# Kernel tuning notes

Measured on AMD Instinct MI355X. Metric: run time of the kernel, lower is better.

Reference implementation:

```python
import jax, jax.numpy as jnp
import numpy as np

B, S, D = 524288, 10, 6  # batch of independent tiny attention problems; original module is one [10,6] sample


def setup_inputs() -> dict:
    key = jax.random.key(0)
    ks = jax.random.split(key, 7)
    bound = 1.0 / np.sqrt(D)  # torch nn.Linear default init range
    x = jax.random.normal(ks[0], (B, S, D), dtype=jnp.float32)
    Wk = jax.random.uniform(ks[1], (D, D), jnp.float32, -bound, bound)
    bk = jax.random.uniform(ks[2], (D,), jnp.float32, -bound, bound)
    Wq = jax.random.uniform(ks[3], (D, D), jnp.float32, -bound, bound)
    bq = jax.random.uniform(ks[4], (D,), jnp.float32, -bound, bound)
    Wv = jax.random.uniform(ks[5], (D, D), jnp.float32, -bound, bound)
    bv = jax.random.uniform(ks[6], (D,), jnp.float32, -bound, bound)
    return {"x": x, "Wk": Wk, "bk": bk, "Wq": Wq, "bq": bq, "Wv": Wv, "bv": bv}


def reference(x, Wk, bk, Wq, bq, Wv, bv):
    # Linear layers (torch stores W as [out,in]; y = x W^T + b)
    k = jnp.einsum('bsd,ed->bse', x, Wk) + bk  # [B,S,D]
    q = jnp.einsum('bsd,ed->bse', x, Wq) + bq
    v = jnp.einsum('bsd,ed->bse', x, Wv) + bv
    # per-query attention over the 10 keys (no scaling in original)
    scores = jax.nn.softmax(jnp.einsum('bqd,bkd->bqk', q, k), axis=-1)  # [B,S,S]
    out = jnp.einsum('bqk,bkd->bqd', scores, v)  # [B,S,D]
    # original sums attended vector over feature dim -> one scalar per query
    return jnp.sum(out, axis=-1)  # [B,S]
```

## Files before the change

kernel.cpp:

```cpp
#include <hip/hip_runtime.h>


#define NB 524288
#define S 10
#define D 6
#define TPB 256
#define EPB 128
#define XFL (S * D)
#define LDS_FLOATS (EPB * XFL)

__global__ void precompute_kernel(const float* __restrict__ Wk, const float* __restrict__ bk,
                                  const float* __restrict__ Wq, const float* __restrict__ bq,
                                  const float* __restrict__ Wv, const float* __restrict__ bv,
                                  float* __restrict__ ws) {
    const float LOG2E = 1.44269504088896340736f;
    int t = threadIdx.x;
    if (t < 36) {
        int d = t / 6, dp = t % 6;
        float g = 0.f;
        for (int e = 0; e < D; ++e) g += Wq[e * D + d] * Wk[e * D + dp];
        ws[t] = g * LOG2E;
    } else if (t < 42) {
        int dp = t - 36;
        float s = 0.f;
        for (int e = 0; e < D; ++e) s += bq[e] * Wk[e * D + dp];
        ws[t] = s * LOG2E;
    } else if (t < 48) {
        int d = t - 42;
        float s = 0.f;
        for (int e = 0; e < D; ++e) s += Wv[e * D + d];
        ws[t] = s;
    } else if (t == 48) {
        float s = 0.f;
        for (int e = 0; e < D; ++e) s += bv[e];
        ws[t] = s;
    }
}

__device__ __forceinline__ float sconst(const float* __restrict__ p, int i) {
    return __int_as_float(__builtin_amdgcn_readfirstlane(__float_as_int(p[i])));
}

__global__ __launch_bounds__(TPB, 4) void attn_kernel(const float* __restrict__ x,
                                                      const float* __restrict__ ws,
                                                      float* __restrict__ out) {
    __shared__ float xs[LDS_FLOATS];
    const int t = threadIdx.x;
    const int blk = blockIdx.x;
    const int wave = t >> 6;
    const int lane = t & 63;

    const float* gbase = x + (size_t)blk * LDS_FLOATS;
    #pragma unroll
    for (int i = 0; i < 8; ++i) {
        int c = wave + 4 * i;
        if (c < 30) {
            __builtin_amdgcn_global_load_lds(
                (const __attribute__((address_space(1))) void*)(gbase + c * 256 + lane * 4),
                (__attribute__((address_space(3))) void*)(&xs[c * 256 + lane * 4]),
                16, 0, 0);
        }
    }

    float G[36], w[6], wvs[6];
    #pragma unroll
    for (int i = 0; i < 36; ++i) G[i] = sconst(ws, i);
    #pragma unroll
    for (int i = 0; i < 6; ++i) w[i] = sconst(ws, 36 + i);
    #pragma unroll
    for (int i = 0; i < 6; ++i) wvs[i] = sconst(ws, 42 + i);
    const float bvs = sconst(ws, 48);

    __syncthreads();

    const int e = t >> 1;
    const int h = t & 1;
    const float* xe = &xs[e * XFL];

    float xv[XFL];
    const float4* xr = (const float4*)xe;
    #pragma unroll
    for (int i = 0; i < 15; ++i) {
        float4 v = xr[i];
        xv[4 * i + 0] = v.x;
        xv[4 * i + 1] = v.y;
        xv[4 * i + 2] = v.z;
        xv[4 * i + 3] = v.w;
    }

    const float* xq0 = xe + h * (5 * D);
    float tq[5][6];
    #pragma unroll
    for (int j = 0; j < 5; ++j) {
        float xq[6];
        #pragma unroll
        for (int d = 0; d < 6; ++d) xq[d] = xq0[j * 6 + d];
        #pragma unroll
        for (int dp = 0; dp < 6; ++dp) {
            float s = 0.f;
            #pragma unroll
            for (int d = 0; d < 6; ++d) s += xq[d] * G[d * 6 + dp];
            tq[j][dp] = s;
        }
    }

    float num[5] = {0.f, 0.f, 0.f, 0.f, 0.f};
    float den[5] = {0.f, 0.f, 0.f, 0.f, 0.f};
    #pragma unroll
    for (int k = 0; k < S; ++k) {
        float a = 0.f, vk = bvs;
        #pragma unroll
        for (int d = 0; d < 6; ++d) {
            a += w[d] * xv[k * 6 + d];
            vk += wvs[d] * xv[k * 6 + d];
        }
        #pragma unroll
        for (int j = 0; j < 5; ++j) {
            float s = a;
            #pragma unroll
            for (int d = 0; d < 6; ++d) s += tq[j][d] * xv[k * 6 + d];
            float ex = __builtin_amdgcn_exp2f(s);
            den[j] += ex;
            num[j] += ex * vk;
        }
    }

    float* op = out + (size_t)blk * (EPB * S) + t * 5;
    #pragma unroll
    for (int j = 0; j < 5; ++j) op[j] = num[j] * __builtin_amdgcn_rcpf(den[j]);
}

extern "C" void kernel_launch(void* const* d_in, const int* in_sizes, int n_in,
                              void* d_out, int out_size, void* d_ws, size_t ws_size,
                              hipStream_t stream) {
    const float* x  = (const float*)d_in[0];
    const float* Wk = (const float*)d_in[1];
    const float* bk = (const float*)d_in[2];
    const float* Wq = (const float*)d_in[3];
    const float* bq = (const float*)d_in[4];
    const float* Wv = (const float*)d_in[5];
    const float* bv = (const float*)d_in[6];
    float* out = (float*)d_out;
    float* ws  = (float*)d_ws;

    precompute_kernel<<<1, 64, 0, stream>>>(Wk, bk, Wq, bq, Wv, bv, ws);
    attn_kernel<<<NB / EPB, TPB, 0, stream>>>(x, ws, out);
}
```

Before: 43.64 us.

## Double-buffer x tiles in LDS across a per-block tile loop and coalesce outputs

Each block now runs 128 threads and loops over 8 tiles of 64 elements. While the current tile is computed, the next tile is prefetched with async global-to-LDS loads into a second buffer, so memory traffic overlaps compute. Results are staged through LDS so each output store is fully coalesced. The grid becomes much smaller (1024 blocks of 2 waves), which lowers occupancy and latency hiding on a kernel that is already close to bandwidth-bound. The loop also adds extra barriers per tile.

After: 45.08 us. +3.3%, slower.

```diff
diff --git a/kernel.cpp b/kernel.cpp
--- a/kernel.cpp
+++ b/kernel.cpp
@@ -4,10 +4,11 @@
 #define NB 524288
 #define S 10
 #define D 6
-#define TPB 256
-#define EPB 128
+#define TPB 128
+#define EPT 64
+#define TILES 8
 #define XFL (S * D)
-#define LDS_FLOATS (EPB * XFL)
+#define TFL (EPT * XFL)
 
 __global__ void precompute_kernel(const float* __restrict__ Wk, const float* __restrict__ bk,
                                   const float* __restrict__ Wq, const float* __restrict__ bq,
@@ -41,26 +42,29 @@
     return __int_as_float(__builtin_amdgcn_readfirstlane(__float_as_int(p[i])));
 }
 
+__device__ __forceinline__ void stage_tile(const float* __restrict__ gsrc,
+                                           float* __restrict__ ldst,
+                                           int wave, int lane) {
+    #pragma unroll
+    for (int i = 0; i < 8; ++i) {
+        int c = wave + 2 * i;
+        if (c < 15) {
+            __builtin_amdgcn_global_load_lds(
+                (const __attribute__((address_space(1))) void*)(gsrc + c * 256 + lane * 4),
+                (__attribute__((address_space(3))) void*)(ldst + c * 256 + lane * 4),
+                16, 0, 0);
+        }
+    }
+}
+
 __global__ __launch_bounds__(TPB, 4) void attn_kernel(const float* __restrict__ x,
                                                       const float* __restrict__ ws,
                                                       float* __restrict__ out) {
-    __shared__ float xs[LDS_FLOATS];
+    __shared__ float xs[2][TFL];
     const int t = threadIdx.x;
-    const int blk = blockIdx.x;
     const int wave = t >> 6;
     const int lane = t & 63;
-
-    const float* gbase = x + (size_t)blk * LDS_FLOATS;
-    #pragma unroll
-    for (int i = 0; i < 8; ++i) {
-        int c = wave + 4 * i;
-        if (c < 30) {
-            __builtin_amdgcn_global_load_lds(
-                (const __attribute__((address_space(1))) void*)(gbase + c * 256 + lane * 4),
-                (__attribute__((address_space(3))) void*)(&xs[c * 256 + lane * 4]),
-                16, 0, 0);
-        }
-    }
+    const int blk = blockIdx.x;
 
     float G[36], w[6], wvs[6];
     #pragma unroll
@@ -71,63 +75,80 @@
     for (int i = 0; i < 6; ++i) wvs[i] = sconst(ws, 42 + i);
     const float bvs = sconst(ws, 48);
 
-    __syncthreads();
+    const float* gbase = x + (size_t)blk * (TILES * TFL);
+    stage_tile(gbase, &xs[0][0], wave, lane);
 
-    const int e = t >> 1;
-    const int h = t & 1;
-    const float* xe = &xs[e * XFL];
+    #pragma unroll 2
+    for (int tt = 0; tt < TILES; ++tt) {
+        __syncthreads();
 
-    float xv[XFL];
-    const float4* xr = (const float4*)xe;
-    #pragma unroll
-    for (int i = 0; i < 15; ++i) {
-        float4 v = xr[i];
-        xv[4 * i + 0] = v.x;
-        xv[4 * i + 1] = v.y;
-        xv[4 * i + 2] = v.z;
-        xv[4 * i + 3] = v.w;
-    }
+        const float* xe = &xs[tt & 1][(t >> 1) * XFL];
 
-    const float* xq0 = xe + h * (5 * D);
-    float tq[5][6];
-    #pragma unroll
-    for (int j = 0; j < 5; ++j) {
-        float xq[6];
+        float xv[XFL];
+        const float4* xr = (const float4*)xe;
         #pragma unroll
-        for (int d = 0; d < 6; ++d) xq[d] = xq0[j * 6 + d];
-        #pragma unroll
-        for (int dp = 0; dp < 6; ++dp) {
-            float s = 0.f;
-            #pragma unroll
-            for (int d = 0; d < 6; ++d) s += xq[d] * G[d * 6 + dp];
-            tq[j][dp] = s;
+        for (int i = 0; i < 15; ++i) {
+            float4 v = xr[i];
+            xv[4 * i + 0] = v.x;
+            xv[4 * i + 1] = v.y;
+            xv[4 * i + 2] = v.z;
+            xv[4 * i + 3] = v.w;
         }
-    }
 
-    float num[5] = {0.f, 0.f, 0.f, 0.f, 0.f};
-    float den[5] = {0.f, 0.f, 0.f, 0.f, 0.f};
-    #pragma unroll
-    for (int k = 0; k < S; ++k) {
-        float a = 0.f, vk = bvs;
-        #pragma unroll
-        for (int d = 0; d < 6; ++d) {
-            a += w[d] * xv[k * 6 + d];
-            vk += wvs[d] * xv[k * 6 + d];
-        }
+        const float* xq0 = xe + (t & 1) * (5 * D);
+        float tq[5][6];
         #pragma unroll
         for (int j = 0; j < 5; ++j) {
-            float s = a;
+            float xq[6];
             #pragma unroll
-            for (int d = 0; d < 6; ++d) s += tq[j][d] * xv[k * 6 + d];
-            float ex = __builtin_amdgcn_exp2f(s);
-            den[j] += ex;
-            num[j] += ex * vk;
+            for (int d = 0; d < 6; ++d) xq[d] = xq0[j * 6 + d];
+            #pragma unroll
+            for (int dp = 0; dp < 6; ++dp) {
+                float s = 0.f;
+                #pragma unroll
+                for (int d = 0; d < 6; ++d) s += xq[d] * G[d * 6 + dp];
+                tq[j][dp] = s;
+            }
         }
+
+        if (tt + 1 < TILES)
+            stage_tile(gbase + (size_t)(tt + 1) * TFL, &xs[(tt + 1) & 1][0], wave, lane);
+
+        float num[5] = {0.f, 0.f, 0.f, 0.f, 0.f};
+        float den[5] = {0.f, 0.f, 0.f, 0.f, 0.f};
+        #pragma unroll
+        for (int k = 0; k < S; ++k) {
+            float a = 0.f, vk = bvs;
+            #pragma unroll
+            for (int d = 0; d < 6; ++d) {
+                a += w[d] * xv[k * 6 + d];
+                vk += wvs[d] * xv[k * 6 + d];
+            }
+            #pragma unroll
+            for (int j = 0; j < 5; ++j) {
+                float s = a;
+                #pragma unroll
+                for (int d = 0; d < 6; ++d) s += tq[j][d] * xv[k * 6 + d];
+                float ex = __builtin_amdgcn_exp2f(s);
+                den[j] += ex;
+                num[j] += ex * vk;
+            }
+        }
+
+        __syncthreads();
+
+        float* os = &xs[tt & 1][0];
+        #pragma unroll
+        for (int j = 0; j < 5; ++j)
+            os[t * 5 + j] = num[j] * __builtin_amdgcn_rcpf(den[j]);
+
+        __syncthreads();
+
+        float* ob = out + (size_t)(blk * TILES + tt) * (EPT * S);
+        #pragma unroll
+        for (int i = 0; i < 5; ++i)
+            ob[i * TPB + t] = os[i * TPB + t];
     }
-
-    float* op = out + (size_t)blk * (EPB * S) + t * 5;
-    #pragma unroll
-    for (int j = 0; j < 5; ++j) op[j] = num[j] * __builtin_amdgcn_rcpf(den[j]);
 }
 
 extern "C" void kernel_launch(void* const* d_in, const int* in_sizes, int n_in,
@@ -144,5 +165,5 @@
     float* ws  = (float*)d_ws;
 
     precompute_kernel<<<1, 64, 0, stream>>>(Wk, bk, Wq, bq, Wv, bv, ws);
-    attn_kernel<<<NB / EPB, TPB, 0, stream>>>(x, ws, out);
+    attn_kernel<<<NB / (EPT * TILES), TPB, 0, stream>>>(x, ws, out);
 }
```

## Fuse weight precompute into attention kernel and halve block size

Applied to the files above, without the earlier changes.

Removes the separate single-block precompute launch. Each block now recomputes the folded Wq·Wk matrix, the bias projection and the Wv sums from the raw weights and pins them to scalar registers. Block size drops to 128 threads covering 64 elements, so there are twice as many blocks and each does a smaller LDS staging. The cost is redundant per-block weight loads and about 250 FMAs per thread, traded against the launch gap and the dependency between two kernels.

Result: slower. 50.38 us (+15.4%).

```diff
diff --git a/kernel.cpp b/kernel.cpp
--- a/kernel.cpp
+++ b/kernel.cpp
@@ -4,57 +4,33 @@
 #define NB 524288
 #define S 10
 #define D 6
-#define TPB 256
-#define EPB 128
+#define TPB 128
+#define EPB 64
 #define XFL (S * D)
 #define LDS_FLOATS (EPB * XFL)
 
-__global__ void precompute_kernel(const float* __restrict__ Wk, const float* __restrict__ bk,
-                                  const float* __restrict__ Wq, const float* __restrict__ bq,
-                                  const float* __restrict__ Wv, const float* __restrict__ bv,
-                                  float* __restrict__ ws) {
-    const float LOG2E = 1.44269504088896340736f;
-    int t = threadIdx.x;
-    if (t < 36) {
-        int d = t / 6, dp = t % 6;
-        float g = 0.f;
-        for (int e = 0; e < D; ++e) g += Wq[e * D + d] * Wk[e * D + dp];
-        ws[t] = g * LOG2E;
-    } else if (t < 42) {
-        int dp = t - 36;
-        float s = 0.f;
-        for (int e = 0; e < D; ++e) s += bq[e] * Wk[e * D + dp];
-        ws[t] = s * LOG2E;
-    } else if (t < 48) {
-        int d = t - 42;
-        float s = 0.f;
-        for (int e = 0; e < D; ++e) s += Wv[e * D + d];
-        ws[t] = s;
-    } else if (t == 48) {
-        float s = 0.f;
-        for (int e = 0; e < D; ++e) s += bv[e];
-        ws[t] = s;
-    }
+__device__ __forceinline__ float pin(float v) {
+    return __int_as_float(__builtin_amdgcn_readfirstlane(__float_as_int(v)));
 }
 
-__device__ __forceinline__ float sconst(const float* __restrict__ p, int i) {
-    return __int_as_float(__builtin_amdgcn_readfirstlane(__float_as_int(p[i])));
-}
-
-__global__ __launch_bounds__(TPB, 4) void attn_kernel(const float* __restrict__ x,
-                                                      const float* __restrict__ ws,
-                                                      float* __restrict__ out) {
+__global__ __launch_bounds__(TPB, 4) void attn_fused(const float* __restrict__ x,
+                                                     const float* __restrict__ Wk,
+                                                     const float* __restrict__ Wq,
+                                                     const float* __restrict__ bq,
+                                                     const float* __restrict__ Wv,
+                                                     const float* __restrict__ bv,
+                                                     float* __restrict__ out) {
     __shared__ float xs[LDS_FLOATS];
     const int t = threadIdx.x;
-    const int blk = blockIdx.x;
     const int wave = t >> 6;
     const int lane = t & 63;
+    const int blk = blockIdx.x;
 
     const float* gbase = x + (size_t)blk * LDS_FLOATS;
     #pragma unroll
     for (int i = 0; i < 8; ++i) {
-        int c = wave + 4 * i;
-        if (c < 30) {
+        int c = wave + 2 * i;
+        if (c < 15) {
             __builtin_amdgcn_global_load_lds(
                 (const __attribute__((address_space(1))) void*)(gbase + c * 256 + lane * 4),
                 (__attribute__((address_space(3))) void*)(&xs[c * 256 + lane * 4]),
@@ -62,19 +38,46 @@
         }
     }
 
+    const float LOG2E = 1.44269504088896340736f;
     float G[36], w[6], wvs[6];
+    {
+        float wq[36], wk[36];
+        #pragma unroll
+        for (int i = 0; i < 36; ++i) wq[i] = Wq[i];
+        #pragma unroll
+        for (int i = 0; i < 36; ++i) wk[i] = Wk[i];
+        #pragma unroll
+        for (int d = 0; d < 6; ++d)
+            #pragma unroll
+            for (int dp = 0; dp < 6; ++dp) {
+                float g = 0.f;
+                #pragma unroll
+                for (int e = 0; e < 6; ++e) g += wq[e * 6 + d] * wk[e * 6 + dp];
+                G[d * 6 + dp] = pin(g * LOG2E);
+            }
+        #pragma unroll
+        for (int dp = 0; dp < 6; ++dp) {
+            float s = 0.f;
+            #pragma unroll
+            for (int e = 0; e < 6; ++e) s += bq[e] * wk[e * 6 + dp];
+            w[dp] = pin(s * LOG2E);
+        }
+        #pragma unroll
+        for (int d = 0; d < 6; ++d) {
+            float s = 0.f;
+            #pragma unroll
+            for (int e = 0; e < 6; ++e) s += Wv[e * 6 + d];
+            wvs[d] = pin(s);
+        }
+    }
+    float bvs = 0.f;
     #pragma unroll
-    for (int i = 0; i < 36; ++i) G[i] = sconst(ws, i);
-    #pragma unroll
-    for (int i = 0; i < 6; ++i) w[i] = sconst(ws, 36 + i);
-    #pragma unroll
-    for (int i = 0; i < 6; ++i) wvs[i] = sconst(ws, 42 + i);
-    const float bvs = sconst(ws, 48);
+    for (int e = 0; e < 6; ++e) bvs += bv[e];
+    bvs = pin(bvs);
 
     __syncthreads();
 
     const int e = t >> 1;
-    const int h = t & 1;
     const float* xe = &xs[e * XFL];
 
     float xv[XFL];
@@ -88,7 +91,7 @@
         xv[4 * i + 3] = v.w;
     }
 
-    const float* xq0 = xe + h * (5 * D);
+    const float* xq0 = xe + (t & 1) * (5 * D);
     float tq[5][6];
     #pragma unroll
     for (int j = 0; j < 5; ++j) {
@@ -135,14 +138,11 @@
                               hipStream_t stream) {
     const float* x  = (const float*)d_in[0];
     const float* Wk = (const float*)d_in[1];
-    const float* bk = (const float*)d_in[2];
     const float* Wq = (const float*)d_in[3];
     const float* bq = (const float*)d_in[4];
     const float* Wv = (const float*)d_in[5];
     const float* bv = (const float*)d_in[6];
     float* out = (float*)d_out;
-    float* ws  = (float*)d_ws;
 
-    precompute_kernel<<<1, 64, 0, stream>>>(Wk, bk, Wq, bq, Wv, bv, ws);
-    attn_kernel<<<NB / EPB, TPB, 0, stream>>>(x, ws, out);
+    attn_fused<<<NB / EPB, TPB, 0, stream>>>(x, Wk, Wq, bq, Wv, bv, out);
 }
```
